# Performance work log

Measured on AMD Instinct MI355X. Metric: run time of the kernel, lower is better.

## Reference

```python
import jax, jax.numpy as jnp
import numpy as np

N, H, W = 4096, 96, 96
C0 = 0.28209479177387814
C1 = 0.4886025119029199
C2 = [1.0925484305920792, -1.0925484305920792, 0.31539156525252005, -1.0925484305920792, 0.5462742152960396]
C3 = [-0.5900435899266435, 2.890611442640554, -0.4570457994644658, 0.3731763325901154, -0.4570457994644658, 1.445305721320277, -0.5900435899266435]


def setup_inputs() -> dict:
    key = jax.random.key(0)
    ks = jax.random.split(key, 6)
    return {
        'pws': jax.random.normal(ks[0], (N, 3), jnp.float32),
        'low_shs': 0.5 * jax.random.normal(ks[1], (N, 3), jnp.float32),
        'high_shs': 0.1 * jax.random.normal(ks[2], (N, 45), jnp.float32),
        'alphas_raw': jax.random.normal(ks[3], (N, 1), jnp.float32),
        'scales_raw': 0.5 * jax.random.normal(ks[4], (N, 3), jnp.float32) - 3.0,
        'rots_raw': jax.random.normal(ks[5], (N, 4), jnp.float32),
        'us': jnp.zeros((N, 2), jnp.float32),
        'Rcw': jnp.eye(3, dtype=jnp.float32),
        'tcw': jnp.array([0.0, 0.0, 4.0], jnp.float32),
        'cam_intr': jnp.array([120.0, 120.0, 48.0, 48.0], jnp.float32),  # fx fy cx cy
    }


def quat_to_rot(q):
    w, x, y, z = q[:, 0], q[:, 1], q[:, 2], q[:, 3]
    return jnp.stack([
        jnp.stack([1 - 2 * (y * y + z * z), 2 * (x * y - w * z), 2 * (x * z + w * y)], -1),
        jnp.stack([2 * (x * y + w * z), 1 - 2 * (x * x + z * z), 2 * (y * z - w * x)], -1),
        jnp.stack([2 * (x * z - w * y), 2 * (y * z + w * x), 1 - 2 * (x * x + y * y)], -1),
    ], -2)  # [N,3,3]


def sh2color(shs, dirs):
    # shs [N,16,3], dirs [N,3] normalized view directions
    x, y, z = dirs[:, 0:1], dirs[:, 1:2], dirs[:, 2:3]
    xx, yy, zz = x * x, y * y, z * z
    xy, yz, xz = x * y, y * z, x * z
    c = C0 * shs[:, 0]
    c = c - C1 * y * shs[:, 1] + C1 * z * shs[:, 2] - C1 * x * shs[:, 3]
    c = (c + C2[0] * xy * shs[:, 4] + C2[1] * yz * shs[:, 5]
         + C2[2] * (2 * zz - xx - yy) * shs[:, 6]
         + C2[3] * xz * shs[:, 7] + C2[4] * (xx - yy) * shs[:, 8])
    c = (c + C3[0] * y * (3 * xx - yy) * shs[:, 9] + C3[1] * xy * z * shs[:, 10]
         + C3[2] * y * (4 * zz - xx - yy) * shs[:, 11]
         + C3[3] * z * (2 * zz - 3 * xx - 3 * yy) * shs[:, 12]
         + C3[4] * x * (4 * zz - xx - yy) * shs[:, 13]
         + C3[5] * z * (xx - yy) * shs[:, 14]
         + C3[6] * x * (xx - 3 * yy) * shs[:, 15])
    return jnp.maximum(c + 0.5, 0.0)  # [N,3]


def _forward(pws, low_shs, high_shs, alphas_raw, scales_raw, rots_raw, Rcw, tcw, cam_intr):
    fx, fy, cx, cy = cam_intr[0], cam_intr[1], cam_intr[2], cam_intr[3]
    alphas = jax.nn.sigmoid(alphas_raw)[:, 0]                 # get_alphas
    scales = jnp.exp(scales_raw)                              # get_scales
    rots = rots_raw / jnp.linalg.norm(rots_raw, axis=1, keepdims=True)  # get_rots
    shs = jnp.concatenate([low_shs, high_shs], axis=1).reshape(-1, 16, 3)

    # --- project ---
    pcs = pws @ Rcw.T + tcw                                   # [N,3] camera coords
    depths = pcs[:, 2]
    zs = jnp.where(depths > 1e-6, depths, 1e-6)
    u = jnp.stack([fx * pcs[:, 0] / zs + cx, fy * pcs[:, 1] / zs + cy], axis=1)

    # --- cov3d = (R S)(R S)^T ---
    M = quat_to_rot(rots) * scales[:, None, :]
    cov3d = M @ jnp.swapaxes(M, 1, 2)                          # [N,3,3]

    # --- cov2d = J W cov3d W^T J^T + 0.3 I ---
    limx, limy = 1.3 * (W / (2.0 * fx)), 1.3 * (H / (2.0 * fy))
    tx = jnp.clip(pcs[:, 0] / zs, -limx, limx) * zs
    ty = jnp.clip(pcs[:, 1] / zs, -limy, limy) * zs
    zero = jnp.zeros_like(zs)
    J = jnp.stack([
        jnp.stack([fx / zs, zero, -fx * tx / (zs * zs)], -1),
        jnp.stack([zero, fy / zs, -fy * ty / (zs * zs)], -1),
    ], -2)                                                     # [N,2,3]
    T = J @ Rcw
    cov2d = T @ cov3d @ jnp.swapaxes(T, 1, 2)
    a = cov2d[:, 0, 0] + 0.3
    b = cov2d[:, 0, 1]
    c2 = cov2d[:, 1, 1] + 0.3

    # --- inverseCov2D + areas (radius of 3-sigma ellipse) ---
    det = a * c2 - b * b
    cinv = jnp.stack([c2, -b, a], axis=1) / det[:, None]       # [N,3]
    mid = 0.5 * (a + c2)
    lam = mid + jnp.sqrt(jnp.maximum(mid * mid - det, 0.1))
    radius = jnp.ceil(3.0 * jnp.sqrt(lam))
    areas = jnp.stack([radius, radius], axis=1)                # [N,2]

    # --- sh2Color ---
    twc = -(Rcw.T @ tcw)
    dirs = pws - twc
    dirs = dirs / jnp.linalg.norm(dirs, axis=1, keepdims=True)
    colors = sh2color(shs, dirs)                               # [N,3]

    # --- splat: depth-sorted alpha compositing ---
    valid = depths > 0.2
    order = jnp.argsort(depths)
    u_s, cinv_s = u[order], cinv[order]
    alpha_s, color_s, valid_s = alphas[order], colors[order], valid[order]

    px = (jnp.arange(W, dtype=jnp.float32))[None, :].repeat(H, 0).reshape(-1)
    py = (jnp.arange(H, dtype=jnp.float32))[:, None].repeat(W, 1).reshape(-1)
    dx = u_s[:, 0:1] - px[None, :]                             # [N,P]
    dy = u_s[:, 1:2] - py[None, :]
    power = -0.5 * (cinv_s[:, 0:1] * dx * dx + cinv_s[:, 2:3] * dy * dy) - cinv_s[:, 1:2] * dx * dy
    ap = jnp.minimum(alpha_s[:, None] * jnp.exp(jnp.minimum(power, 0.0)), 0.99)
    ap = jnp.where((ap >= 1.0 / 255.0) & valid_s[:, None], ap, 0.0)
    logt = jnp.cumsum(jnp.log1p(-ap), axis=0)
    tau = jnp.exp(jnp.concatenate([jnp.zeros((1, ap.shape[1])), logt[:-1]], axis=0))
    wgt = jnp.where(tau > 1e-4, ap * tau, 0.0)                 # [N,P]
    image = jnp.einsum('nc,np->cp', color_s, wgt).reshape(3, H, W)
    return image, areas


def reference(pws, low_shs, high_shs, alphas_raw, scales_raw, rots_raw, us, Rcw, tcw, cam_intr):
    return _forward(pws, low_shs, high_shs, alphas_raw, scales_raw, rots_raw, Rcw, tcw, cam_intr)
```

## Files before the change

### kernel.cpp

```cpp
#include <hip/hip_runtime.h>
#include <hip/hip_bf16.h>
#include <math.h>

#define GS_N 4096
#define IMG_H 96
#define IMG_W 96
#define NPIX (IMG_H * IMG_W)
#define TILE_PX 12
#define TILES_X 8
#define NTILES (TILES_X * TILES_X)
#define WAVES_PER_TILE 36

#define SH_C0 0.28209479177387814f
#define SH_C1 0.4886025119029199f
__device__ __constant__ float kC2[5] = {1.0925484305920792f, -1.0925484305920792f, 0.31539156525252005f, -1.0925484305920792f, 0.5462742152960396f};
__device__ __constant__ float kC3[7] = {-0.5900435899266435f, 2.890611442640554f, -0.4570457994644658f, 0.3731763325901154f, -0.4570457994644658f, 1.445305721320277f, -0.5900435899266435f};

__global__ __launch_bounds__(256) void gs_prep(
    const float* __restrict__ pws, const float* __restrict__ low_shs,
    const float* __restrict__ high_shs, const float* __restrict__ alphas_raw,
    const float* __restrict__ scales_raw, const float* __restrict__ rots_raw,
    const float* __restrict__ Rcw, const float* __restrict__ tcw,
    const float* __restrict__ cam,
    float* __restrict__ areas_out,
    float* __restrict__ depth_ws,
    int*   __restrict__ rank_ws,
    float4* __restrict__ A_uns,
    float4* __restrict__ B_uns,
    float* __restrict__ C_uns,
    float4* __restrict__ D_uns,
    unsigned long long* __restrict__ mask_ws)
{
    int i = blockIdx.x * 256 + threadIdx.x;
    if (i >= GS_N) return;

    rank_ws[i] = 0;
    mask_ws[i] = 0ull;

    float fx = cam[0], fy = cam[1], cxi = cam[2], cyi = cam[3];
    float R0 = Rcw[0], R1 = Rcw[1], R2 = Rcw[2];
    float R3 = Rcw[3], R4 = Rcw[4], R5 = Rcw[5];
    float R6 = Rcw[6], R7 = Rcw[7], R8 = Rcw[8];
    float t0 = tcw[0], t1 = tcw[1], t2 = tcw[2];

    float pwx = pws[3*i+0], pwy = pws[3*i+1], pwz = pws[3*i+2];

    float pcx = R0*pwx + R1*pwy + R2*pwz + t0;
    float pcy = R3*pwx + R4*pwy + R5*pwz + t1;
    float pcz = R6*pwx + R7*pwy + R8*pwz + t2;

    float depth = pcz;
    float zs = (depth > 1e-6f) ? depth : 1e-6f;

    float ux = fx * pcx / zs + cxi;
    float uy = fy * pcy / zs + cyi;

    float alpha = 1.0f / (1.0f + expf(-alphas_raw[i]));

    float s0 = expf(scales_raw[3*i+0]);
    float s1 = expf(scales_raw[3*i+1]);
    float s2 = expf(scales_raw[3*i+2]);

    float qw = rots_raw[4*i+0], qx = rots_raw[4*i+1], qy = rots_raw[4*i+2], qz = rots_raw[4*i+3];
    float qn = sqrtf(qw*qw + qx*qx + qy*qy + qz*qz);
    qw /= qn; qx /= qn; qy /= qn; qz /= qn;

    float r00 = 1.0f - 2.0f*(qy*qy + qz*qz);
    float r01 = 2.0f*(qx*qy - qw*qz);
    float r02 = 2.0f*(qx*qz + qw*qy);
    float r10 = 2.0f*(qx*qy + qw*qz);
    float r11 = 1.0f - 2.0f*(qx*qx + qz*qz);
    float r12 = 2.0f*(qy*qz - qw*qx);
    float r20 = 2.0f*(qx*qz - qw*qy);
    float r21 = 2.0f*(qy*qz + qw*qx);
    float r22 = 1.0f - 2.0f*(qx*qx + qy*qy);

    float m00 = r00*s0, m01 = r01*s1, m02 = r02*s2;
    float m10 = r10*s0, m11 = r11*s1, m12 = r12*s2;
    float m20 = r20*s0, m21 = r21*s1, m22 = r22*s2;

    float V00 = m00*m00 + m01*m01 + m02*m02;
    float V01 = m00*m10 + m01*m11 + m02*m12;
    float V02 = m00*m20 + m01*m21 + m02*m22;
    float V11 = m10*m10 + m11*m11 + m12*m12;
    float V12 = m10*m20 + m11*m21 + m12*m22;
    float V22 = m20*m20 + m21*m21 + m22*m22;

    float limx = 1.3f * ((float)IMG_W / (2.0f * fx));
    float limy = 1.3f * ((float)IMG_H / (2.0f * fy));
    float xzr = pcx / zs, yzr = pcy / zs;
    float txv = fminf(fmaxf(xzr, -limx), limx) * zs;
    float tyv = fminf(fmaxf(yzr, -limy), limy) * zs;

    float J00 = fx / zs, J02 = -fx * txv / (zs * zs);
    float J11 = fy / zs, J12 = -fy * tyv / (zs * zs);

    float T00 = J00*R0 + J02*R6, T01 = J00*R1 + J02*R7, T02 = J00*R2 + J02*R8;
    float T10 = J11*R3 + J12*R6, T11 = J11*R4 + J12*R7, T12 = J11*R5 + J12*R8;

    float TW00 = T00*V00 + T01*V01 + T02*V02;
    float TW01 = T00*V01 + T01*V11 + T02*V12;
    float TW02 = T00*V02 + T01*V12 + T02*V22;
    float TW10 = T10*V00 + T11*V01 + T12*V02;
    float TW11 = T10*V01 + T11*V11 + T12*V12;
    float TW12 = T10*V02 + T11*V12 + T12*V22;

    float c00 = TW00*T00 + TW01*T01 + TW02*T02;
    float c01 = TW00*T10 + TW01*T11 + TW02*T12;
    float c11 = TW10*T10 + TW11*T11 + TW12*T12;

    float a  = c00 + 0.3f;
    float b  = c01;
    float cc = c11 + 0.3f;
    float det = a * cc - b * b;
    float ci0 = cc / det;
    float ci1 = -b / det;
    float ci2 = a / det;

    float mid = 0.5f * (a + cc);
    float lam = mid + sqrtf(fmaxf(mid * mid - det, 0.1f));
    float radius = ceilf(3.0f * sqrtf(lam));
    areas_out[2*i + 0] = radius;
    areas_out[2*i + 1] = radius;

    float twcx = -(R0*t0 + R3*t1 + R6*t2);
    float twcy = -(R1*t0 + R4*t1 + R7*t2);
    float twcz = -(R2*t0 + R5*t1 + R8*t2);
    float dx = pwx - twcx, dy = pwy - twcy, dz = pwz - twcz;
    float dn = sqrtf(dx*dx + dy*dy + dz*dz);
    dx /= dn; dy /= dn; dz /= dn;

    float xx = dx*dx, yy = dy*dy, zz = dz*dz;
    float xy = dx*dy, yz = dy*dz, xz = dx*dz;

    float bas0  = SH_C0;
    float bas1  = -SH_C1 * dy;
    float bas2  =  SH_C1 * dz;
    float bas3  = -SH_C1 * dx;
    float bas4  = kC2[0] * xy;
    float bas5  = kC2[1] * yz;
    float bas6  = kC2[2] * (2.0f*zz - xx - yy);
    float bas7  = kC2[3] * xz;
    float bas8  = kC2[4] * (xx - yy);
    float bas9  = kC3[0] * dy * (3.0f*xx - yy);
    float bas10 = kC3[1] * xy * dz;
    float bas11 = kC3[2] * dy * (4.0f*zz - xx - yy);
    float bas12 = kC3[3] * dz * (2.0f*zz - 3.0f*xx - 3.0f*yy);
    float bas13 = kC3[4] * dx * (4.0f*zz - xx - yy);
    float bas14 = kC3[5] * dz * (xx - yy);
    float bas15 = kC3[6] * dx * (xx - 3.0f*yy);

    float col[3];
    #pragma unroll
    for (int c = 0; c < 3; ++c) {
        const float* hs = high_shs + 45*i + c;
        float acc = bas0 * low_shs[3*i + c];
        acc += bas1  * hs[0*3];
        acc += bas2  * hs[1*3];
        acc += bas3  * hs[2*3];
        acc += bas4  * hs[3*3];
        acc += bas5  * hs[4*3];
        acc += bas6  * hs[5*3];
        acc += bas7  * hs[6*3];
        acc += bas8  * hs[7*3];
        acc += bas9  * hs[8*3];
        acc += bas10 * hs[9*3];
        acc += bas11 * hs[10*3];
        acc += bas12 * hs[11*3];
        acc += bas13 * hs[12*3];
        acc += bas14 * hs[13*3];
        acc += bas15 * hs[14*3];
        col[c] = fmaxf(acc + 0.5f, 0.0f);
    }

    bool valid = depth > 0.2f;
    float al_eff = valid ? alpha : 0.0f;

    float Tthr = __logf(255.0f * al_eff) + 1e-4f;
    float rx = (Tthr > 0.0f) ? sqrtf(2.0f * Tthr * a)  : -1.0f;
    float ry = (Tthr > 0.0f) ? sqrtf(2.0f * Tthr * cc) : -1.0f;

    depth_ws[i] = depth;
    A_uns[i] = make_float4(ux, uy, ci0, ci1);
    B_uns[i] = make_float4(ci2, al_eff, col[0], col[1]);
    C_uns[i] = col[2];
    D_uns[i] = make_float4(ux, uy, rx, ry);
}

__global__ __launch_bounds__(256) void gs_rank_partial(
    const float* __restrict__ depth, int* __restrict__ rank_ws)
{
    __shared__ float sd[256];
    int itile = blockIdx.x >> 4;
    int jtile = blockIdx.x & 15;
    int tid = threadIdx.x;
    int i = itile * 256 + tid;

    sd[tid] = depth[jtile * 256 + tid];
    __syncthreads();

    float mg = depth[i];
    int jbase = jtile * 256;
    int rank = 0;
    const float4* s4 = (const float4*)sd;
    #pragma unroll 16
    for (int jj = 0; jj < 64; ++jj) {
        float4 v = s4[jj];
        int j0 = jbase + jj * 4;
        rank += (v.x < mg || (v.x == mg && (j0+0) < i)) ? 1 : 0;
        rank += (v.y < mg || (v.y == mg && (j0+1) < i)) ? 1 : 0;
        rank += (v.z < mg || (v.z == mg && (j0+2) < i)) ? 1 : 0;
        rank += (v.w < mg || (v.w == mg && (j0+3) < i)) ? 1 : 0;
    }
    atomicAdd(&rank_ws[i], rank);
}

__global__ __launch_bounds__(256) void gs_gather_mask(
    const int* __restrict__ rank_ws,
    const float4* __restrict__ A_uns, const float4* __restrict__ B_uns,
    const float* __restrict__ C_uns, const float4* __restrict__ D_uns,
    float4* __restrict__ A_s, float4* __restrict__ B_s, float* __restrict__ C_s,
    unsigned long long* __restrict__ mask_ws)
{
    int i = blockIdx.x * 256 + threadIdx.x;
    int r = rank_ws[i];
    A_s[r] = A_uns[i];
    B_s[r] = B_uns[i];
    C_s[r] = C_uns[i];

    float4 d = D_uns[i];
    if (d.z >= 0.0f) {
        const float inv = 1.0f / (float)TILE_PX;
        int tx0 = max(0, (int)ceilf((d.x - d.z - (float)(TILE_PX - 1)) * inv - 1e-4f));
        int tx1 = min(TILES_X - 1, (int)floorf((d.x + d.z) * inv + 1e-4f));
        int ty0 = max(0, (int)ceilf((d.y - d.w - (float)(TILE_PX - 1)) * inv - 1e-4f));
        int ty1 = min(TILES_X - 1, (int)floorf((d.y + d.w) * inv + 1e-4f));
        unsigned long long bit = 1ull << (r & 63);
        int w = r >> 6;
        for (int ty = ty0; ty <= ty1; ++ty)
            for (int tx = tx0; tx <= tx1; ++tx)
                atomicOr(&mask_ws[(ty * TILES_X + tx) * 64 + w], bit);
    }
}

__global__ __launch_bounds__(256) void gs_expand(
    const unsigned long long* __restrict__ mask_ws,
    const float4* __restrict__ A_s, const float4* __restrict__ B_s,
    const float* __restrict__ C_s,
    float4* __restrict__ E_A, float4* __restrict__ E_B, float* __restrict__ E_C,
    int* __restrict__ tile_cnt)
{
    __shared__ unsigned short slist[GS_N];
    __shared__ int scnt;

    int tile = blockIdx.x;
    int tid = threadIdx.x;
    int lane = tid & 63, wv = tid >> 6;

    if (wv == 0) {
        unsigned long long m = mask_ws[tile * 64 + lane];
        int c = __popcll(m);
        int incl = c;
        #pragma unroll
        for (int d = 1; d < 64; d <<= 1) {
            int v = __shfl_up(incl, d, 64);
            if (lane >= d) incl += v;
        }
        int off = incl - c;
        int base = lane << 6;
        while (m) {
            int bpos = __builtin_ctzll(m);
            m &= m - 1;
            slist[off++] = (unsigned short)(base + bpos);
        }
        if (lane == 63) { scnt = incl; tile_cnt[tile] = incl; }
    }
    __syncthreads();
    int cnt = scnt;

    float4* tA = E_A + tile * GS_N;
    float4* tB = E_B + tile * GS_N;
    float*  tC = E_C + tile * GS_N;
    for (int k = tid; k < cnt; k += 256) {
        int n = slist[k];
        tA[k] = A_s[n];
        tB[k] = B_s[n];
        tC[k] = C_s[n];
    }
}

__global__ __launch_bounds__(256) void gs_raster(
    const float4* __restrict__ E_A, const float4* __restrict__ E_B,
    const float* __restrict__ E_C,
    const int* __restrict__ tile_cnt,
    float* __restrict__ img)
{
    int b = blockIdx.x;
    int tile = b / WAVES_PER_TILE;
    int sub  = b - tile * WAVES_PER_TILE;
    int lane = threadIdx.x & 63;
    int wv   = threadIdx.x >> 6;

    int idxp = sub * 4 + wv;
    int lx = idxp % TILE_PX, ly = idxp / TILE_PX;
    int tx = tile & (TILES_X - 1), ty = tile >> 3;
    int pxi = tx * TILE_PX + lx, pyi = ty * TILE_PX + ly;
    float px = (float)pxi, py = (float)pyi;
    int p = pyi * IMG_W + pxi;

    int cnt = tile_cnt[tile];
    const float4* tA = E_A + tile * GS_N;
    const float4* tB = E_B + tile * GS_N;
    const float*  tC = E_C + tile * GS_N;

    float carry = 1.0f;
    float accr = 0.0f, accg = 0.0f, accb = 0.0f;

    for (int c0 = 0; c0 < cnt; c0 += 64) {
        int k = c0 + lane;
        float ap = 0.0f, colr = 0.0f, colg = 0.0f, colb = 0.0f;
        if (k < cnt) {
            float4 a4 = tA[k];
            float4 b4 = tB[k];
            colb = tC[k];
            colr = b4.z; colg = b4.w;

            float ddx = a4.x - px;
            float ddy = a4.y - py;
            float pw = -0.5f * (a4.z * ddx * ddx + b4.x * ddy * ddy) - a4.w * ddx * ddy;
            pw = fminf(pw, 0.0f);
            ap = b4.y * __expf(pw);
            ap = fminf(ap, 0.99f);
            ap = (ap >= (1.0f / 255.0f)) ? ap : 0.0f;
        }

        if (__ballot(ap > 0.0f) == 0ull) continue;

        float f = 1.0f - ap;
        float incl = f;
        #pragma unroll
        for (int d = 1; d < 64; d <<= 1) {
            float v = __shfl_up(incl, d, 64);
            if (lane >= d) incl *= v;
        }
        float excl = __shfl_up(incl, 1, 64);
        if (lane == 0) excl = 1.0f;

        float tau = carry * excl;
        float wgt = (tau > 1e-4f) ? ap * tau : 0.0f;
        accr += colr * wgt;
        accg += colg * wgt;
        accb += colb * wgt;

        carry *= __shfl(incl, 63, 64);
        if (carry <= 1e-4f) break;
    }

    #pragma unroll
    for (int d = 32; d >= 1; d >>= 1) {
        accr += __shfl_xor(accr, d, 64);
        accg += __shfl_xor(accg, d, 64);
        accb += __shfl_xor(accb, d, 64);
    }
    if (lane == 0) {
        img[0 * NPIX + p] = accr;
        img[1 * NPIX + p] = accg;
        img[2 * NPIX + p] = accb;
    }
}

extern "C" void kernel_launch(void* const* d_in, const int* in_sizes, int n_in,
                              void* d_out, int out_size, void* d_ws, size_t ws_size,
                              hipStream_t stream) {
    const float* pws        = (const float*)d_in[0];
    const float* low_shs    = (const float*)d_in[1];
    const float* high_shs   = (const float*)d_in[2];
    const float* alphas_raw = (const float*)d_in[3];
    const float* scales_raw = (const float*)d_in[4];
    const float* rots_raw   = (const float*)d_in[5];
    const float* Rcw        = (const float*)d_in[7];
    const float* tcw        = (const float*)d_in[8];
    const float* cam        = (const float*)d_in[9];

    float* out_img   = (float*)d_out;
    float* out_areas = (float*)d_out + 3 * NPIX;

    char* ws = (char*)d_ws;
    float*  depth_ws = (float*) (ws + 0);
    int*    rank_ws  = (int*)   (ws + 16384);
    float4* A_uns    = (float4*)(ws + 32768);
    float4* B_uns    = (float4*)(ws + 98304);
    float*  C_uns    = (float*) (ws + 163840);
    float4* D_uns    = (float4*)(ws + 180224);
    float4* A_s      = (float4*)(ws + 245760);
    float4* B_s      = (float4*)(ws + 311296);
    float*  C_s      = (float*) (ws + 376832);
    unsigned long long* mask_ws = (unsigned long long*)(ws + 393216);
    float4* E_A      = (float4*)(ws + 425984);
    float4* E_B      = (float4*)(ws + 4620288);
    float*  E_C      = (float*) (ws + 8814592);
    int*    tile_cnt = (int*)   (ws + 9863168);

    gs_prep<<<GS_N / 256, 256, 0, stream>>>(
        pws, low_shs, high_shs, alphas_raw, scales_raw, rots_raw, Rcw, tcw, cam,
        out_areas, depth_ws, rank_ws, A_uns, B_uns, C_uns, D_uns, mask_ws);

    gs_rank_partial<<<256, 256, 0, stream>>>(depth_ws, rank_ws);

    gs_gather_mask<<<GS_N / 256, 256, 0, stream>>>(
        rank_ws, A_uns, B_uns, C_uns, D_uns, A_s, B_s, C_s, mask_ws);

    gs_expand<<<NTILES, 256, 0, stream>>>(
        mask_ws, A_s, B_s, C_s, E_A, E_B, E_C, tile_cnt);

    gs_raster<<<NTILES * WAVES_PER_TILE, 256, 0, stream>>>(
        E_A, E_B, E_C, tile_cnt, out_img);
}
```

Before: 95.05 us.

## Process two splats per lane with DPP prefix product and drop sorted copies

The raster loop now handles 128 splats per wave iteration, two per lane. It multiplies their transmittances before a single wave-wide inclusive product scan, which is built from DPP row shifts and row broadcasts instead of shuffle loops. The gather kernel no longer scatters the A/B/C arrays into sorted order. It writes an inverse permutation, and the expand kernel reads the unsorted data through it. This cuts scan overhead and one copy pass, at the cost of strided per-lane loads and an extra indirection in expand.

```diff
diff --git a/kernel.cpp b/kernel.cpp
--- a/kernel.cpp
+++ b/kernel.cpp
@@ -15,6 +15,34 @@
 #define SH_C1 0.4886025119029199f
 __device__ __constant__ float kC2[5] = {1.0925484305920792f, -1.0925484305920792f, 0.31539156525252005f, -1.0925484305920792f, 0.5462742152960396f};
 __device__ __constant__ float kC3[7] = {-0.5900435899266435f, 2.890611442640554f, -0.4570457994644658f, 0.3731763325901154f, -0.4570457994644658f, 1.445305721320277f, -0.5900435899266435f};
+
+__device__ __forceinline__ float wave_incl_prod(float x) {
+#if __has_builtin(__builtin_amdgcn_update_dpp)
+    const int ONE = __float_as_int(1.0f);
+    int t;
+    t = __builtin_amdgcn_update_dpp(ONE, __float_as_int(x), 0x111, 0xf, 0xf, false);
+    x *= __int_as_float(t);
+    t = __builtin_amdgcn_update_dpp(ONE, __float_as_int(x), 0x112, 0xf, 0xf, false);
+    x *= __int_as_float(t);
+    t = __builtin_amdgcn_update_dpp(ONE, __float_as_int(x), 0x114, 0xf, 0xf, false);
+    x *= __int_as_float(t);
+    t = __builtin_amdgcn_update_dpp(ONE, __float_as_int(x), 0x118, 0xf, 0xf, false);
+    x *= __int_as_float(t);
+    t = __builtin_amdgcn_update_dpp(ONE, __float_as_int(x), 0x142, 0xa, 0xf, false);
+    x *= __int_as_float(t);
+    t = __builtin_amdgcn_update_dpp(ONE, __float_as_int(x), 0x143, 0xc, 0xf, false);
+    x *= __int_as_float(t);
+    return x;
+#else
+    int lane = threadIdx.x & 63;
+    #pragma unroll
+    for (int d = 1; d < 64; d <<= 1) {
+        float v = __shfl_up(x, d, 64);
+        if (lane >= d) x *= v;
+    }
+    return x;
+#endif
+}
 
 __global__ __launch_bounds__(256) void gs_prep(
     const float* __restrict__ pws, const float* __restrict__ low_shs,
@@ -217,16 +245,13 @@
 
 __global__ __launch_bounds__(256) void gs_gather_mask(
     const int* __restrict__ rank_ws,
-    const float4* __restrict__ A_uns, const float4* __restrict__ B_uns,
-    const float* __restrict__ C_uns, const float4* __restrict__ D_uns,
-    float4* __restrict__ A_s, float4* __restrict__ B_s, float* __restrict__ C_s,
+    const float4* __restrict__ D_uns,
+    int* __restrict__ inv_ws,
     unsigned long long* __restrict__ mask_ws)
 {
     int i = blockIdx.x * 256 + threadIdx.x;
     int r = rank_ws[i];
-    A_s[r] = A_uns[i];
-    B_s[r] = B_uns[i];
-    C_s[r] = C_uns[i];
+    inv_ws[r] = i;
 
     float4 d = D_uns[i];
     if (d.z >= 0.0f) {
@@ -245,8 +270,9 @@
 
 __global__ __launch_bounds__(256) void gs_expand(
     const unsigned long long* __restrict__ mask_ws,
-    const float4* __restrict__ A_s, const float4* __restrict__ B_s,
-    const float* __restrict__ C_s,
+    const int* __restrict__ inv_ws,
+    const float4* __restrict__ A_uns, const float4* __restrict__ B_uns,
+    const float* __restrict__ C_uns,
     float4* __restrict__ E_A, float4* __restrict__ E_B, float* __restrict__ E_C,
     int* __restrict__ tile_cnt)
 {
@@ -282,10 +308,10 @@
     float4* tB = E_B + tile * GS_N;
     float*  tC = E_C + tile * GS_N;
     for (int k = tid; k < cnt; k += 256) {
-        int n = slist[k];
-        tA[k] = A_s[n];
-        tB[k] = B_s[n];
-        tC[k] = C_s[n];
+        int n = inv_ws[slist[k]];
+        tA[k] = A_uns[n];
+        tB[k] = B_uns[n];
+        tC[k] = C_uns[n];
     }
 }
 
@@ -316,41 +342,48 @@
     float carry = 1.0f;
     float accr = 0.0f, accg = 0.0f, accb = 0.0f;
 
-    for (int c0 = 0; c0 < cnt; c0 += 64) {
-        int k = c0 + lane;
-        float ap = 0.0f, colr = 0.0f, colg = 0.0f, colb = 0.0f;
-        if (k < cnt) {
-            float4 a4 = tA[k];
-            float4 b4 = tB[k];
-            colb = tC[k];
-            colr = b4.z; colg = b4.w;
-
-            float ddx = a4.x - px;
-            float ddy = a4.y - py;
+    for (int c0 = 0; c0 < cnt; c0 += 128) {
+        int k0 = c0 + (lane << 1);
+        float ap0 = 0.0f, r0 = 0.0f, g0 = 0.0f, b0 = 0.0f;
+        float ap1 = 0.0f, r1 = 0.0f, g1 = 0.0f, b1 = 0.0f;
+        if (k0 < cnt) {
+            float4 a4 = tA[k0];
+            float4 b4 = tB[k0];
+            b0 = tC[k0]; r0 = b4.z; g0 = b4.w;
+            float ddx = a4.x - px, ddy = a4.y - py;
             float pw = -0.5f * (a4.z * ddx * ddx + b4.x * ddy * ddy) - a4.w * ddx * ddy;
             pw = fminf(pw, 0.0f);
-            ap = b4.y * __expf(pw);
-            ap = fminf(ap, 0.99f);
-            ap = (ap >= (1.0f / 255.0f)) ? ap : 0.0f;
+            ap0 = b4.y * __expf(pw);
+            ap0 = fminf(ap0, 0.99f);
+            ap0 = (ap0 >= (1.0f / 255.0f)) ? ap0 : 0.0f;
         }
-
-        if (__ballot(ap > 0.0f) == 0ull) continue;
-
-        float f = 1.0f - ap;
-        float incl = f;
-        #pragma unroll
-        for (int d = 1; d < 64; d <<= 1) {
-            float v = __shfl_up(incl, d, 64);
-            if (lane >= d) incl *= v;
+        if (k0 + 1 < cnt) {
+            float4 a4 = tA[k0 + 1];
+            float4 b4 = tB[k0 + 1];
+            b1 = tC[k0 + 1]; r1 = b4.z; g1 = b4.w;
+            float ddx = a4.x - px, ddy = a4.y - py;
+            float pw = -0.5f * (a4.z * ddx * ddx + b4.x * ddy * ddy) - a4.w * ddx * ddy;
+            pw = fminf(pw, 0.0f);
+            ap1 = b4.y * __expf(pw);
+            ap1 = fminf(ap1, 0.99f);
+            ap1 = (ap1 >= (1.0f / 255.0f)) ? ap1 : 0.0f;
         }
+
+        if (__ballot(ap0 > 0.0f || ap1 > 0.0f) == 0ull) continue;
+
+        float f0 = 1.0f - ap0;
+        float f1 = 1.0f - ap1;
+        float incl = wave_incl_prod(f0 * f1);
         float excl = __shfl_up(incl, 1, 64);
-        if (lane == 0) excl = 1.0f;
-
-        float tau = carry * excl;
-        float wgt = (tau > 1e-4f) ? ap * tau : 0.0f;
-        accr += colr * wgt;
-        accg += colg * wgt;
-        accb += colb * wgt;
+        excl = (lane == 0) ? 1.0f : excl;
+
+        float tau0 = carry * excl;
+        float tau1 = tau0 * f0;
+        float w0 = (tau0 > 1e-4f) ? ap0 * tau0 : 0.0f;
+        float w1 = (tau1 > 1e-4f) ? ap1 * tau1 : 0.0f;
+        accr += r0 * w0 + r1 * w1;
+        accg += g0 * w0 + g1 * w1;
+        accb += b0 * w0 + b1 * w1;
 
         carry *= __shfl(incl, 63, 64);
         if (carry <= 1e-4f) break;
@@ -388,18 +421,16 @@
     char* ws = (char*)d_ws;
     float*  depth_ws = (float*) (ws + 0);
     int*    rank_ws  = (int*)   (ws + 16384);
-    float4* A_uns    = (float4*)(ws + 32768);
-    float4* B_uns    = (float4*)(ws + 98304);
-    float*  C_uns    = (float*) (ws + 163840);
-    float4* D_uns    = (float4*)(ws + 180224);
-    float4* A_s      = (float4*)(ws + 245760);
-    float4* B_s      = (float4*)(ws + 311296);
-    float*  C_s      = (float*) (ws + 376832);
-    unsigned long long* mask_ws = (unsigned long long*)(ws + 393216);
-    float4* E_A      = (float4*)(ws + 425984);
-    float4* E_B      = (float4*)(ws + 4620288);
-    float*  E_C      = (float*) (ws + 8814592);
-    int*    tile_cnt = (int*)   (ws + 9863168);
+    int*    inv_ws   = (int*)   (ws + 32768);
+    float4* A_uns    = (float4*)(ws + 49152);
+    float4* B_uns    = (float4*)(ws + 114688);
+    float*  C_uns    = (float*) (ws + 180224);
+    float4* D_uns    = (float4*)(ws + 196608);
+    unsigned long long* mask_ws = (unsigned long long*)(ws + 262144);
+    float4* E_A      = (float4*)(ws + 294912);
+    float4* E_B      = (float4*)(ws + 4489216);
+    float*  E_C      = (float*) (ws + 8683520);
+    int*    tile_cnt = (int*)   (ws + 9732096);
 
     gs_prep<<<GS_N / 256, 256, 0, stream>>>(
         pws, low_shs, high_shs, alphas_raw, scales_raw, rots_raw, Rcw, tcw, cam,
@@ -408,10 +439,10 @@
     gs_rank_partial<<<256, 256, 0, stream>>>(depth_ws, rank_ws);
 
     gs_gather_mask<<<GS_N / 256, 256, 0, stream>>>(
-        rank_ws, A_uns, B_uns, C_uns, D_uns, A_s, B_s, C_s, mask_ws);
+        rank_ws, D_uns, inv_ws, mask_ws);
 
     gs_expand<<<NTILES, 256, 0, stream>>>(
-        mask_ws, A_s, B_s, C_s, E_A, E_B, E_C, tile_cnt);
+        mask_ws, inv_ws, A_uns, B_uns, C_uns, E_A, E_B, E_C, tile_cnt);
 
     gs_raster<<<NTILES * WAVES_PER_TILE, 256, 0, stream>>>(
         E_A, E_B, E_C, tile_cnt, out_img);
```

Result: no change. 94.76 us (median of 2 runs) (-0.3%).
